# Kernel optimization log

Hardware: AMD Instinct MI355X
Metric: run time of the kernel (lower is better)

## Reference

```python
import jax, jax.numpy as jnp
import numpy as np

B, S, D, H, DFF, L, V = 256, 77, 512, 8, 2048, 12, 49408
HD = D // H
EPS = 1e-5


def setup_inputs() -> dict:
    key = jax.random.key(0)
    ks = jax.random.split(key, 12)
    s = 0.02
    n = lambda k, shape: s * jax.random.normal(k, shape, dtype=jnp.float32)
    return {
        "input_ids": jax.random.randint(ks[0], (B, S), 0, V),
        "attention_mask": jnp.ones((B, S), dtype=jnp.int32),
        "tok_emb": n(ks[1], (V, D)),
        "pos_emb": n(ks[2], (S, D)),
        "ln1_w": jnp.ones((L, D)), "ln1_b": jnp.zeros((L, D)),
        "q_w": n(ks[3], (L, D, D)), "q_b": jnp.zeros((L, D)),
        "k_w": n(ks[4], (L, D, D)), "k_b": jnp.zeros((L, D)),
        "v_w": n(ks[5], (L, D, D)), "v_b": jnp.zeros((L, D)),
        "o_w": n(ks[6], (L, D, D)), "o_b": jnp.zeros((L, D)),
        "ln2_w": jnp.ones((L, D)), "ln2_b": jnp.zeros((L, D)),
        "fc1_w": n(ks[7], (L, DFF, D)), "fc1_b": jnp.zeros((L, DFF)),
        "fc2_w": n(ks[8], (L, D, DFF)), "fc2_b": jnp.zeros((L, D)),
        "lnf_w": jnp.ones((D,)), "lnf_b": jnp.zeros((D,)),
    }


def layer_norm(x, w, b):
    mu = jnp.mean(x, axis=-1, keepdims=True)
    var = jnp.mean(jnp.square(x - mu), axis=-1, keepdims=True)
    return (x - mu) * jax.lax.rsqrt(var + EPS) * w + b


def quick_gelu(x):
    return x * jax.nn.sigmoid(1.702 * x)


def _encoder(x, mask, layer_params):
    scale = HD ** -0.5

    def heads(t):  # [B,S,D] -> [B,H,S,HD]
        return t.reshape(B, S, H, HD).transpose(0, 2, 1, 3)

    def layer(x, p):
        (ln1w, ln1b, qw, qb, kw, kb, vw, vb, ow, ob,
         ln2w, ln2b, f1w, f1b, f2w, f2b) = p
        h = layer_norm(x, ln1w, ln1b)
        q = heads((h @ qw.T + qb) * scale)
        k = heads(h @ kw.T + kb)
        v = heads(h @ vw.T + vb)
        scores = jnp.einsum('bhqd,bhkd->bhqk', q, k) + mask
        probs = jax.nn.softmax(scores, axis=-1)
        a = jnp.einsum('bhqk,bhkd->bhqd', probs, v)
        a = a.transpose(0, 2, 1, 3).reshape(B, S, D) @ ow.T + ob
        x = x + a
        h = layer_norm(x, ln2w, ln2b)
        h = quick_gelu(h @ f1w.T + f1b)
        h = h @ f2w.T + f2b
        return x + h, None

    x, _ = jax.lax.scan(layer, x, layer_params)
    return x


def reference(input_ids, attention_mask, tok_emb, pos_emb,
              ln1_w, ln1_b, q_w, q_b, k_w, k_b, v_w, v_b, o_w, o_b,
              ln2_w, ln2_b, fc1_w, fc1_b, fc2_w, fc2_b, lnf_w, lnf_b):
    x = tok_emb[input_ids] + pos_emb[None]
    neg = jnp.finfo(x.dtype).min
    causal = jnp.triu(jnp.full((S, S), neg, x.dtype), k=1)[None, None]  # [1,1,S,S]
    pad = (1.0 - attention_mask.astype(x.dtype))[:, None, None, :] * neg  # [B,1,1,S]
    mask = causal + pad  # [B,1,S,S]
    layer_params = (ln1_w, ln1_b, q_w, q_b, k_w, k_b, v_w, v_b, o_w, o_b,
                    ln2_w, ln2_b, fc1_w, fc1_b, fc2_w, fc2_b)
    x = _encoder(x, mask, layer_params)
    last_hidden = layer_norm(x, lnf_w, lnf_b)
    # pooled output: eot token = argmax of input_ids (CLIP convention)
    pooled = last_hidden[jnp.arange(B), jnp.argmax(input_ids, axis=-1)]
    return last_hidden, pooled
```

## Files before the change

kernel.cpp:

```cpp
#include <hip/hip_runtime.h>
#include <math.h>

constexpr int BATCH  = 256;
constexpr int SEQ    = 77;
constexpr int DMODEL = 512;
constexpr int NHEAD  = 8;
constexpr int DHEAD  = 64;
constexpr int DFF    = 2048;
constexpr int NLAYER = 12;
constexpr int NTOK   = BATCH * SEQ;
constexpr int NQKV   = 3 * DMODEL;
constexpr float NEGBIG = -3.402823466e38f;

typedef __attribute__((ext_vector_type(8))) short bf16x8;
typedef __attribute__((ext_vector_type(4))) float f32x4;
typedef __attribute__((ext_vector_type(8))) unsigned short u16x8;

typedef __attribute__((address_space(3))) unsigned char lds_u8;
typedef const __attribute__((address_space(1))) unsigned char g_u8;

__device__ __forceinline__ unsigned short f2bf(float f) {
    unsigned u = __float_as_uint(f);
    u = (u + 0x7FFF + ((u >> 16) & 1)) >> 16;
    return (unsigned short)u;
}

#define VMCNT4 asm volatile("s_waitcnt vmcnt(4)" ::: "memory")
#define LGKM0  asm volatile("s_waitcnt lgkmcnt(0)" ::: "memory")
#define SCHEDB __builtin_amdgcn_sched_barrier(0)
#define BARRIER do { SCHEDB; __builtin_amdgcn_s_barrier(); SCHEDB; } while (0)

__global__ __launch_bounds__(256) void conv_qkv_kernel(
    const float* __restrict__ qw, const float* __restrict__ kw,
    const float* __restrict__ vw, unsigned short* __restrict__ dst)
{
    int i4 = blockIdx.x * 256 + threadIdx.x;
    int e = i4 * 4;
    int l = e / (NQKV * DMODEL);
    int rem = e - l * (NQKV * DMODEL);
    int row = rem >> 9;
    int k   = rem & 511;
    const float* src;
    float scale = 1.0f;
    size_t lbase = (size_t)l * DMODEL * DMODEL;
    if (row < 512)       { src = qw + lbase + (size_t)row * DMODEL + k; scale = 0.125f; }
    else if (row < 1024) { src = kw + lbase + (size_t)(row - 512) * DMODEL + k; }
    else                 { src = vw + lbase + (size_t)(row - 1024) * DMODEL + k; }
    float4 v = *(const float4*)src;
    ushort4 o;
    o.x = f2bf(v.x * scale); o.y = f2bf(v.y * scale);
    o.z = f2bf(v.z * scale); o.w = f2bf(v.w * scale);
    *(ushort4*)&dst[e] = o;
}

__global__ __launch_bounds__(256) void conv_kernel(
    const float* __restrict__ src, unsigned short* __restrict__ dst)
{
    int e = (blockIdx.x * 256 + threadIdx.x) * 4;
    float4 v = *(const float4*)&src[e];
    ushort4 o;
    o.x = f2bf(v.x); o.y = f2bf(v.y); o.z = f2bf(v.z); o.w = f2bf(v.w);
    *(ushort4*)&dst[e] = o;
}

__global__ __launch_bounds__(256) void bias_qkv_kernel(
    const float* __restrict__ qb, const float* __restrict__ kb,
    const float* __restrict__ vb, float* __restrict__ dst)
{
    int e = blockIdx.x * 256 + threadIdx.x;
    int l = e / NQKV;
    int row = e - l * NQKV;
    float v;
    if (row < 512)       v = qb[l * DMODEL + row] * 0.125f;
    else if (row < 1024) v = kb[l * DMODEL + row - 512];
    else                 v = vb[l * DMODEL + row - 1024];
    dst[e] = v;
}

__global__ __launch_bounds__(256) void embed_kernel(
    const int* __restrict__ ids, const float* __restrict__ tok,
    const float* __restrict__ pos, float* __restrict__ x)
{
    int f = blockIdx.x * 256 + threadIdx.x;
    int total = NTOK * (DMODEL / 4);
    if (f >= total) return;
    int n  = f >> 7;
    int d4 = f & 127;
    int s  = n % SEQ;
    int id = ids[n];
    float4 t = *(const float4*)&tok[(size_t)id * DMODEL + d4 * 4];
    float4 p = *(const float4*)&pos[(size_t)s  * DMODEL + d4 * 4];
    float4 o; o.x = t.x + p.x; o.y = t.y + p.y; o.z = t.z + p.z; o.w = t.w + p.w;
    *(float4*)&x[(size_t)n * DMODEL + d4 * 4] = o;
}

template <bool BF16OUT>
__global__ __launch_bounds__(256) void ln_kernel(
    const float* __restrict__ x, const float* __restrict__ w,
    const float* __restrict__ b, void* __restrict__ out, int nrows)
{
    int row = blockIdx.x * 4 + (threadIdx.x >> 6);
    if (row >= nrows) return;
    int ln = threadIdx.x & 63;
    const float* xr = x + (size_t)row * DMODEL + ln * 8;
    float4 v0 = *(const float4*)xr;
    float4 v1 = *(const float4*)(xr + 4);
    float va[8] = {v0.x, v0.y, v0.z, v0.w, v1.x, v1.y, v1.z, v1.w};
    float sum = 0.f, sq = 0.f;
#pragma unroll
    for (int j = 0; j < 8; ++j) { sum += va[j]; sq = fmaf(va[j], va[j], sq); }
#pragma unroll
    for (int o = 32; o; o >>= 1) { sum += __shfl_xor(sum, o); sq += __shfl_xor(sq, o); }
    float mu  = sum * (1.0f / DMODEL);
    float var = sq * (1.0f / DMODEL) - mu * mu;
    var = fmaxf(var, 0.0f);
    float inv = 1.0f / sqrtf(var + 1e-5f);
    const float* wp = w + ln * 8;
    const float* bp = b + ln * 8;
    float o8[8];
#pragma unroll
    for (int j = 0; j < 8; ++j) o8[j] = (va[j] - mu) * inv * wp[j] + bp[j];
    if (BF16OUT) {
        u16x8 pk;
#pragma unroll
        for (int j = 0; j < 8; ++j) pk[j] = f2bf(o8[j]);
        *(u16x8*)((unsigned short*)out + (size_t)row * DMODEL + ln * 8) = pk;
    } else {
        float* op = (float*)out + (size_t)row * DMODEL + ln * 8;
        *(float4*)op       = make_float4(o8[0], o8[1], o8[2], o8[3]);
        *(float4*)(op + 4) = make_float4(o8[4], o8[5], o8[6], o8[7]);
    }
}

template <int MODE, bool OUTBF>
__global__ __launch_bounds__(512, 2) void gemm8_bf16(
    const unsigned short* __restrict__ A, const unsigned short* __restrict__ W,
    const float* __restrict__ bias, const float* __restrict__ R,
    void* __restrict__ Cout, int M, int N, int K, int gx)
{
    __shared__ __align__(16) char lds[131072];
    const int nwg = gridDim.x;
    const int wg  = blockIdx.x;
    const int q8  = nwg >> 3, r8 = nwg & 7;
    const int xcd = wg & 7, pos = wg >> 3;
    const int start = (xcd < r8) ? xcd * (q8 + 1) : r8 * (q8 + 1) + (xcd - r8) * q8;
    const int newid = start + pos;
    const int by = newid / gx;
    const int bx = newid - by * gx;
    const int m0 = by * 256;
    const int n0 = bx * 256;

    const int tid  = threadIdx.x;
    const int wid  = tid >> 6;
    const int lane = tid & 63;
    const int wr   = wid >> 2;
    const int wc   = wid & 3;
    const int lhi  = lane >> 4;
    const int llo  = lane & 15;

    const int srow  = tid >> 3;
    const int cglob = (tid & 7) ^ (srow & 7);
    const unsigned short* Ap = A + (size_t)(m0 + srow) * K + cglob * 8;
    const unsigned short* Wp = W + (size_t)(n0 + srow) * K + cglob * 8;
    const int NT  = K >> 6;
    const int NT2 = K >> 7;

    const int cb0 = ((0 * 4 + lhi) ^ (llo & 7)) * 16;
    const int cb1 = ((1 * 4 + lhi) ^ (llo & 7)) * 16;
    const int rbA0 = (wr * 128 + 0 * 64 + llo) * 128;
    const int rbA1 = (wr * 128 + 1 * 64 + llo) * 128;
    const int rbB0 = (wc * 64 + 0 * 32 + llo) * 128;
    const int rbB1 = (wc * 64 + 1 * 32 + llo) * 128;

    f32x4 acc[8][4];
#pragma unroll
    for (int i = 0; i < 8; ++i)
#pragma unroll
        for (int j = 0; j < 4; ++j) acc[i][j] = (f32x4){0.f, 0.f, 0.f, 0.f};

    bf16x8 am[4][2], bn0[2][2], bn1[2][2];

    auto stA = [&](int b, int h, int kt) {
#pragma unroll
        for (int i = h * 2; i < h * 2 + 2; ++i)
            __builtin_amdgcn_global_load_lds(
                (g_u8*)(Ap + (size_t)i * 64 * K + kt * 64),
                (lds_u8*)(lds + b * 32768 + i * 8192 + wid * 1024), 16, 0, 0);
    };
    auto stB = [&](int b, int h, int kt) {
#pragma unroll
        for (int i = h * 2; i < h * 2 + 2; ++i)
            __builtin_amdgcn_global_load_lds(
                (g_u8*)(Wp + (size_t)i * 64 * K + kt * 64),
                (lds_u8*)(lds + 65536 + b * 32768 + i * 8192 + wid * 1024), 16, 0, 0);
    };
    auto rdA = [&](int b, int mh) {
        int base = b * 32768 + (mh ? rbA1 : rbA0);
#pragma unroll
        for (int fm = 0; fm < 4; ++fm) {
            am[fm][0] = *(const bf16x8*)(lds + base + fm * 2048 + cb0);
            am[fm][1] = *(const bf16x8*)(lds + base + fm * 2048 + cb1);
        }
    };
    auto rdB = [&](int b, int nh, bf16x8 (&bn)[2][2]) {
        int base = 65536 + b * 32768 + (nh ? rbB1 : rbB0);
#pragma unroll
        for (int fn = 0; fn < 2; ++fn) {
            bn[fn][0] = *(const bf16x8*)(lds + base + fn * 2048 + cb0);
            bn[fn][1] = *(const bf16x8*)(lds + base + fn * 2048 + cb1);
        }
    };
    auto mq = [&](int mh, int nh, bf16x8 (&bn)[2][2]) {
        __builtin_amdgcn_s_setprio(1);
#pragma unroll
        for (int fm = 0; fm < 4; ++fm)
#pragma unroll
            for (int fn = 0; fn < 2; ++fn)
#pragma unroll
                for (int ks = 0; ks < 2; ++ks)
                    acc[mh * 4 + fm][nh * 2 + fn] =
                        __builtin_amdgcn_mfma_f32_16x16x32_bf16(
                            am[fm][ks], bn[fn][ks], acc[mh * 4 + fm][nh * 2 + fn], 0, 0, 0);
        __builtin_amdgcn_s_setprio(0);
    };

    stA(0, 0, 0); stA(0, 1, 0);
    stB(0, 0, 0); stB(0, 1, 0);
    stB(1, 0, 1); stB(1, 1, 1);
    VMCNT4;
    BARRIER;

    for (int it = 0; it < NT2; ++it) {
        const int k1 = 2 * it + 1;
        const int k2 = (2 * it + 2 < NT) ? 2 * it + 2 : NT - 1;
        const int k3 = (2 * it + 3 < NT) ? 2 * it + 3 : NT - 1;
        rdA(0, 0); rdB(0, 0, bn0);
        stA(1, 0, k1);
        LGKM0; BARRIER;
        mq(0, 0, bn0);
        rdB(0, 1, bn1);
        stA(1, 1, k1);
        LGKM0; BARRIER;
        mq(0, 1, bn1);
        rdA(0, 1);
        stB(0, 0, k2);
        LGKM0; BARRIER;
        mq(1, 1, bn1);
        stB(0, 1, k2);
        VMCNT4; BARRIER;
        mq(1, 0, bn0);
        rdA(1, 0); rdB(1, 0, bn0);
        stA(0, 0, k2);
        LGKM0; BARRIER;
        mq(0, 0, bn0);
        rdB(1, 1, bn1);
        stA(0, 1, k2);
        LGKM0; BARRIER;
        mq(0, 1, bn1);
        rdA(1, 1);
        stB(1, 0, k3);
        LGKM0; BARRIER;
        mq(1, 1, bn1);
        stB(1, 1, k3);
        VMCNT4; BARRIER;
        mq(1, 0, bn0);
    }

    if (OUTBF) {
        unsigned short* sb = (unsigned short*)lds;
#pragma unroll
        for (int j = 0; j < 4; ++j) {
            int colL = wc * 64 + j * 16 + llo;
            float bv = bias[n0 + colL];
#pragma unroll
            for (int i = 0; i < 8; ++i) {
                int rowL = wr * 128 + i * 16 + lhi * 4;
#pragma unroll
                for (int r = 0; r < 4; ++r) {
                    float o = acc[i][j][r] + bv;
                    if (MODE == 2) o = o / (1.0f + __expf(-1.702f * o));
                    sb[(rowL + r) * 256 + colL] = f2bf(o);
                }
            }
        }
        __syncthreads();
        const int l5 = lane & 31, lh2 = lane >> 5;
#pragma unroll
        for (int rr = 0; rr < 16; ++rr) {
            int rowL = rr * 16 + wid * 2 + lh2;
            u16x8 v = *(const u16x8*)&sb[rowL * 256 + l5 * 8];
            *(u16x8*)((unsigned short*)Cout + (size_t)(m0 + rowL) * N + n0 + l5 * 8) = v;
        }
    } else {
        float* sf = (float*)lds;
#pragma unroll
        for (int mh = 0; mh < 2; ++mh) {
            if (mh) __syncthreads();
            if (wr == mh) {
#pragma unroll
                for (int j = 0; j < 4; ++j) {
                    int colL = wc * 64 + j * 16 + llo;
                    float bv = bias[n0 + colL];
#pragma unroll
                    for (int i = 0; i < 8; ++i) {
                        int rowL = i * 16 + lhi * 4;
#pragma unroll
                        for (int r = 0; r < 4; ++r)
                            sf[(rowL + r) * 256 + colL] = acc[i][j][r] + bv;
                    }
                }
            }
            __syncthreads();
#pragma unroll
            for (int rr = 0; rr < 16; ++rr) {
                int rowL = rr * 8 + wid;
                size_t gidx = (size_t)(m0 + mh * 128 + rowL) * N + n0 + lane * 4;
                f32x4 v = *(const f32x4*)&sf[rowL * 256 + lane * 4];
                if (MODE == 3) {
                    f32x4 rv = *(const f32x4*)&R[gidx];
                    v = v + rv;
                }
                *(f32x4*)((float*)Cout + gidx) = v;
            }
        }
    }
}

__global__ __launch_bounds__(256) void attn_mfma_kernel(
    const unsigned short* __restrict__ qkv, const int* __restrict__ amask,
    unsigned short* __restrict__ out)
{
    const int bh = blockIdx.x;
    const int b = bh >> 3;
    const int h = bh & 7;
    __shared__ __align__(16) char smem[68160];
    char* Qs = smem;
    char* Ks = smem + 10240;
    char* Vt = smem;
    char* Pb = smem + 20480;
    float* ss = (float*)(smem + 40960);
    float* padm = (float*)(smem + 67840);
    const int tid  = threadIdx.x;
    const int wid  = tid >> 6;
    const int lane = tid & 63;
    const int llo  = lane & 15;
    const int lhi  = lane >> 4;

    for (int f = tid; f < 640; f += 256) {
        int r = f >> 3, c = f & 7;
        bf16x8 pq, pk;
        if (r < SEQ) {
            size_t g = ((size_t)(b * SEQ + r)) * NQKV + h * DHEAD + c * 8;
            pq = *(const bf16x8*)&qkv[g];
            pk = *(const bf16x8*)&qkv[g + 512];
        } else {
#pragma unroll
            for (int j = 0; j < 8; ++j) { pq[j] = 0; pk[j] = 0; }
        }
        int byte = r * 128 + ((c * 16) ^ ((r & 7) << 4));
        *(bf16x8*)(Qs + byte) = pq;
        *(bf16x8*)(Ks + byte) = pk;
    }
    for (int s = tid; s < SEQ; s += 256)
        padm[s] = (1.0f - (float)amask[b * SEQ + s]) * NEGBIG;
    __syncthreads();

    for (int t = wid; t < 25; t += 4) {
        int rt = t / 5, ct = t % 5;
        int ar = rt * 16 + llo;
        int br = ct * 16 + llo;
        int aswz = (ar & 7) << 4;
        int bswz = (br & 7) << 4;
        bf16x8 a0 = *(const bf16x8*)(Qs + ar * 128 + ((lhi * 16) ^ aswz));
        bf16x8 a1 = *(const bf16x8*)(Qs + ar * 128 + (((lhi + 4) * 16) ^ aswz));
        bf16x8 b0 = *(const bf16x8*)(Ks + br * 128 + ((lhi * 16) ^ bswz));
        bf16x8 b1 = *(const bf16x8*)(Ks + br * 128 + (((lhi + 4) * 16) ^ bswz));
        f32x4 acc = (f32x4){0.f, 0.f, 0.f, 0.f};
        acc = __builtin_amdgcn_mfma_f32_16x16x32_bf16(a0, b0, acc, 0, 0, 0);
        acc = __builtin_amdgcn_mfma_f32_16x16x32_bf16(a1, b1, acc, 0, 0, 0);
        int ki = ct * 16 + llo;
#pragma unroll
        for (int r = 0; r < 4; ++r) {
            int qi = rt * 16 + lhi * 4 + r;
            ss[qi * 84 + ki] = (ki > qi || ki >= SEQ) ? NEGBIG : (acc[r] + padm[ki]);
        }
    }
    __syncthreads();

    for (int f = tid; f < SEQ * 8; f += 256) {
        int s = f >> 3, d8 = (f & 7) * 8;
        bf16x8 v = *(const bf16x8*)&qkv[((size_t)(b * SEQ + s)) * NQKV + 1024 + h * DHEAD + d8];
        int chunk16 = (s >> 3) * 16, within = (s & 7) * 2;
#pragma unroll
        for (int j = 0; j < 8; ++j) {
            int d = d8 + j;
            int byte = d * 256 + (chunk16 ^ ((d & 7) << 4)) + within;
            *(short*)(Vt + byte) = v[j];
        }
    }
    for (int f = tid; f < 64 * 19; f += 256) {
        int d = f & 63, s = 77 + (f >> 6);
        int byte = d * 256 + (((s >> 3) * 16) ^ ((d & 7) << 4)) + (s & 7) * 2;
        *(short*)(Vt + byte) = 0;
    }

    for (int qi = wid; qi < SEQ; qi += 4) {
        float s0 = ss[qi * 84 + lane];
        float s1 = (lane < 16) ? ss[qi * 84 + 64 + lane] : NEGBIG;
        float m = fmaxf(s0, s1);
#pragma unroll
        for (int o = 32; o; o >>= 1) m = fmaxf(m, __shfl_xor(m, o));
        float e0 = __expf(s0 - m);
        float e1 = (lane < 16) ? __expf(s1 - m) : 0.f;
        float tsum = e0 + e1;
#pragma unroll
        for (int o = 32; o; o >>= 1) tsum += __shfl_xor(tsum, o);
        float rinv = 1.0f / tsum;
        int qswz = (qi & 7) << 4;
        {
            int col = lane;
            int byte = qi * 256 + (((col >> 3) * 16) ^ qswz) + (col & 7) * 2;
            *(short*)(Pb + byte) = (short)f2bf(e0 * rinv);
        }
        if (lane < 32) {
            int col = 64 + lane;
            float p = (lane < 16) ? e1 * rinv : 0.f;
            int byte = qi * 256 + (((col >> 3) * 16) ^ qswz) + (col & 7) * 2;
            *(short*)(Pb + byte) = (short)f2bf(p);
        }
    }
    __syncthreads();

    for (int t = wid; t < 20; t += 4) {
        int rt = t >> 2, ct = t & 3;
        int ar = rt * 16 + llo;
        int br = ct * 16 + llo;
        int aswz = (ar & 7) << 4;
        int bswz = (br & 7) << 4;
        f32x4 acc = (f32x4){0.f, 0.f, 0.f, 0.f};
#pragma unroll
        for (int kc = 0; kc < 3; ++kc) {
            bf16x8 af  = *(const bf16x8*)(Pb + ar * 256 + (((kc * 4 + lhi) * 16) ^ aswz));
            bf16x8 bf_ = *(const bf16x8*)(Vt + br * 256 + (((kc * 4 + lhi) * 16) ^ bswz));
            acc = __builtin_amdgcn_mfma_f32_16x16x32_bf16(af, bf_, acc, 0, 0, 0);
        }
        int d = ct * 16 + llo;
#pragma unroll
        for (int r = 0; r < 4; ++r) {
            int qi = rt * 16 + lhi * 4 + r;
            if (qi < SEQ)
                out[((size_t)(b * SEQ + qi)) * DMODEL + h * DHEAD + d] = f2bf(acc[r]);
        }
    }
}

__global__ __launch_bounds__(64) void pool_kernel(
    const int* __restrict__ ids, const float* __restrict__ lh,
    float* __restrict__ pooled)
{
    int b = blockIdx.x;
    int ln = threadIdx.x;
    __shared__ int sidx;
    if (ln == 0) {
        int best = ids[b * SEQ]; int bi = 0;
        for (int s = 1; s < SEQ; ++s) {
            int vv = ids[b * SEQ + s];
            if (vv > best) { best = vv; bi = s; }
        }
        sidx = bi;
    }
    __syncthreads();
    const float* src = lh + ((size_t)(b * SEQ + sidx)) * DMODEL + ln * 8;
    float* dst = pooled + (size_t)b * DMODEL + ln * 8;
    float4 a = *(const float4*)src;
    float4 c = *(const float4*)(src + 4);
    *(float4*)dst       = a;
    *(float4*)(dst + 4) = c;
}

extern "C" void kernel_launch(void* const* d_in, const int* in_sizes, int n_in,
                              void* d_out, int out_size, void* d_ws, size_t ws_size,
                              hipStream_t stream) {
    const int*   ids   = (const int*)d_in[0];
    const int*   amask = (const int*)d_in[1];
    const float* tok   = (const float*)d_in[2];
    const float* pos   = (const float*)d_in[3];
    const float* ln1w  = (const float*)d_in[4];
    const float* ln1b  = (const float*)d_in[5];
    const float* qw    = (const float*)d_in[6];
    const float* qbias = (const float*)d_in[7];
    const float* kw    = (const float*)d_in[8];
    const float* kbias = (const float*)d_in[9];
    const float* vw    = (const float*)d_in[10];
    const float* vbias = (const float*)d_in[11];
    const float* ow    = (const float*)d_in[12];
    const float* obias = (const float*)d_in[13];
    const float* ln2w  = (const float*)d_in[14];
    const float* ln2b  = (const float*)d_in[15];
    const float* f1w   = (const float*)d_in[16];
    const float* f1b   = (const float*)d_in[17];
    const float* f2w   = (const float*)d_in[18];
    const float* f2b   = (const float*)d_in[19];
    const float* lnfw  = (const float*)d_in[20];
    const float* lnfb  = (const float*)d_in[21];

    char* p = (char*)d_ws;
    float* x = (float*)p;                      p += (size_t)NTOK * DMODEL * 4;
    unsigned short* hbuf = (unsigned short*)p; p += (size_t)NTOK * DMODEL * 2;
    unsigned short* qkvb = (unsigned short*)p; p += (size_t)NTOK * NQKV * 2;
    unsigned short* ao = (unsigned short*)p;   p += (size_t)NTOK * DMODEL * 2;
    unsigned short* ff = (unsigned short*)p;   p += (size_t)NTOK * DFF * 2;
    unsigned short* wqkv = (unsigned short*)p; p += (size_t)NLAYER * NQKV * DMODEL * 2;
    unsigned short* wo   = (unsigned short*)p; p += (size_t)NLAYER * DMODEL * DMODEL * 2;
    unsigned short* wf1  = (unsigned short*)p; p += (size_t)NLAYER * DFF * DMODEL * 2;
    unsigned short* wf2  = (unsigned short*)p; p += (size_t)NLAYER * DMODEL * DFF * 2;
    float* bqkv = (float*)p;                   p += (size_t)NLAYER * NQKV * 4;

    conv_qkv_kernel<<<(NLAYER * NQKV * DMODEL / 4) / 256, 256, 0, stream>>>(qw, kw, vw, wqkv);
    conv_kernel<<<(NLAYER * DMODEL * DMODEL / 4) / 256, 256, 0, stream>>>(ow, wo);
    conv_kernel<<<(NLAYER * DFF * DMODEL / 4) / 256, 256, 0, stream>>>(f1w, wf1);
    conv_kernel<<<(NLAYER * DMODEL * DFF / 4) / 256, 256, 0, stream>>>(f2w, wf2);
    bias_qkv_kernel<<<(NLAYER * NQKV) / 256, 256, 0, stream>>>(qbias, kbias, vbias, bqkv);

    embed_kernel<<<(NTOK * (DMODEL / 4) + 255) / 256, 256, 0, stream>>>(ids, tok, pos, x);

    const int MB = NTOK / 256;
    dim3 gqkv(MB * (NQKV / 256));
    dim3 g512(MB * (DMODEL / 256));
    dim3 g2048(MB * (DFF / 256));

    for (int l = 0; l < NLAYER; ++l) {
        const size_t wD2 = (size_t)l * DMODEL * DMODEL;
        const size_t wDF = (size_t)l * DFF * DMODEL;
        const size_t oD  = (size_t)l * DMODEL;
        const size_t oF  = (size_t)l * DFF;

        ln_kernel<true><<<NTOK / 4, 256, 0, stream>>>(x, ln1w + oD, ln1b + oD, hbuf, NTOK);
        gemm8_bf16<0, true><<<gqkv, 512, 0, stream>>>(
            hbuf, wqkv + (size_t)l * NQKV * DMODEL, bqkv + (size_t)l * NQKV, nullptr,
            qkvb, NTOK, NQKV, DMODEL, NQKV / 256);
        attn_mfma_kernel<<<BATCH * NHEAD, 256, 0, stream>>>(qkvb, amask, ao);
        gemm8_bf16<3, false><<<g512, 512, 0, stream>>>(
            ao, wo + wD2, obias + oD, x, x, NTOK, DMODEL, DMODEL, DMODEL / 256);
        ln_kernel<true><<<NTOK / 4, 256, 0, stream>>>(x, ln2w + oD, ln2b + oD, hbuf, NTOK);
        gemm8_bf16<2, true><<<g2048, 512, 0, stream>>>(
            hbuf, wf1 + wDF, f1b + oF, nullptr, ff, NTOK, DFF, DMODEL, DFF / 256);
        gemm8_bf16<3, false><<<g512, 512, 0, stream>>>(
            ff, wf2 + wDF, f2b + oD, x, x, NTOK, DMODEL, DFF, DMODEL / 256);
    }

    float* outf = (float*)d_out;
    ln_kernel<false><<<NTOK / 4, 256, 0, stream>>>(x, lnfw, lnfb, outf, NTOK);
    pool_kernel<<<BATCH, 64, 0, stream>>>(ids, outf, outf + (size_t)NTOK * DMODEL);
}
```

Before: 3.759 ms.

## Prefetch V into registers early and widen softmax to four rows per wave

The attention kernel now issues the global loads for the V head slice at kernel entry into registers, so their latency overlaps the Q/K staging and the QK^T MFMA phase. The loads are written into the transposed LDS layout only after the score barrier. The softmax now handles four rows per wave, with 16 lanes per row and five columns per lane, which cuts the shuffle reductions per row. The explicit zeroing of V padding rows is replaced by zeroing the padded P columns 80-95 instead. This relies on the stale LDS contents under Vt staying finite, and it raises register pressure from holding three V vectors across the first phase.

```diff
diff --git a/kernel.cpp b/kernel.cpp
--- a/kernel.cpp
+++ b/kernel.cpp
@@ -346,6 +346,24 @@
     const int llo  = lane & 15;
     const int lhi  = lane >> 4;
 
+    const size_t vbase = ((size_t)(b * SEQ)) * NQKV + 1024 + h * DHEAD;
+    bf16x8 vr0, vr1, vr2;
+    {
+        int c0 = tid, c1 = tid + 256, c2 = tid + 512;
+        vr0 = *(const bf16x8*)&qkv[vbase + (size_t)(c0 >> 3) * NQKV + (c0 & 7) * 8];
+        vr1 = *(const bf16x8*)&qkv[vbase + (size_t)(c1 >> 3) * NQKV + (c1 & 7) * 8];
+        if (c2 < 616)
+            vr2 = *(const bf16x8*)&qkv[vbase + (size_t)(c2 >> 3) * NQKV + (c2 & 7) * 8];
+    }
+
+    if (tid < 160) {
+        int r = tid >> 1, ch = 10 + (tid & 1);
+        bf16x8 z;
+#pragma unroll
+        for (int j = 0; j < 8; ++j) z[j] = 0;
+        *(bf16x8*)(Pb + r * 256 + ((ch ^ (r & 7)) * 16)) = z;
+    }
+
     for (int f = tid; f < 640; f += 256) {
         int r = f >> 3, c = f & 7;
         bf16x8 pq, pk;
@@ -387,46 +405,50 @@
     }
     __syncthreads();
 
-    for (int f = tid; f < SEQ * 8; f += 256) {
-        int s = f >> 3, d8 = (f & 7) * 8;
-        bf16x8 v = *(const bf16x8*)&qkv[((size_t)(b * SEQ + s)) * NQKV + 1024 + h * DHEAD + d8];
-        int chunk16 = (s >> 3) * 16, within = (s & 7) * 2;
-#pragma unroll
-        for (int j = 0; j < 8; ++j) {
-            int d = d8 + j;
-            int byte = d * 256 + (chunk16 ^ ((d & 7) << 4)) + within;
-            *(short*)(Vt + byte) = v[j];
-        }
-    }
-    for (int f = tid; f < 64 * 19; f += 256) {
-        int d = f & 63, s = 77 + (f >> 6);
-        int byte = d * 256 + (((s >> 3) * 16) ^ ((d & 7) << 4)) + (s & 7) * 2;
-        *(short*)(Vt + byte) = 0;
-    }
-
-    for (int qi = wid; qi < SEQ; qi += 4) {
-        float s0 = ss[qi * 84 + lane];
-        float s1 = (lane < 16) ? ss[qi * 84 + 64 + lane] : NEGBIG;
-        float m = fmaxf(s0, s1);
-#pragma unroll
-        for (int o = 32; o; o >>= 1) m = fmaxf(m, __shfl_xor(m, o));
-        float e0 = __expf(s0 - m);
-        float e1 = (lane < 16) ? __expf(s1 - m) : 0.f;
-        float tsum = e0 + e1;
-#pragma unroll
-        for (int o = 32; o; o >>= 1) tsum += __shfl_xor(tsum, o);
-        float rinv = 1.0f / tsum;
-        int qswz = (qi & 7) << 4;
-        {
-            int col = lane;
-            int byte = qi * 256 + (((col >> 3) * 16) ^ qswz) + (col & 7) * 2;
-            *(short*)(Pb + byte) = (short)f2bf(e0 * rinv);
-        }
-        if (lane < 32) {
-            int col = 64 + lane;
-            float p = (lane < 16) ? e1 * rinv : 0.f;
-            int byte = qi * 256 + (((col >> 3) * 16) ^ qswz) + (col & 7) * 2;
-            *(short*)(Pb + byte) = (short)f2bf(p);
+    {
+        auto writeV = [&](int c, bf16x8 v) {
+            int s = c >> 3, d8 = (c & 7) * 8;
+            int chunk16 = (s >> 3) * 16, within = (s & 7) * 2;
+#pragma unroll
+            for (int j = 0; j < 8; ++j) {
+                int d = d8 + j;
+                *(short*)(Vt + d * 256 + (chunk16 ^ ((d & 7) << 4)) + within) = v[j];
+            }
+        };
+        writeV(tid, vr0);
+        writeV(tid + 256, vr1);
+        if (tid + 512 < 616) writeV(tid + 512, vr2);
+    }
+
+    {
+        const int g = lane >> 4;
+        const int c = lane & 15;
+#pragma unroll
+        for (int pass = 0; pass < 5; ++pass) {
+            int r = pass * 16 + wid * 4 + g;
+            float v0 = ss[r * 84 + c];
+            float v1 = ss[r * 84 + c + 16];
+            float v2 = ss[r * 84 + c + 32];
+            float v3 = ss[r * 84 + c + 48];
+            float v4 = ss[r * 84 + c + 64];
+            float m = fmaxf(fmaxf(fmaxf(v0, v1), fmaxf(v2, v3)), v4);
+#pragma unroll
+            for (int o = 8; o; o >>= 1) m = fmaxf(m, __shfl_xor(m, o));
+            float e0 = __expf(v0 - m), e1 = __expf(v1 - m), e2 = __expf(v2 - m);
+            float e3 = __expf(v3 - m), e4 = __expf(v4 - m);
+            float tsum = e0 + e1 + e2 + e3 + e4;
+#pragma unroll
+            for (int o = 8; o; o >>= 1) tsum += __shfl_xor(tsum, o);
+            float rinv = 1.0f / tsum;
+            int rswz = (r & 7) << 4;
+            int rb = r * 256;
+            float ev[5] = {e0, e1, e2, e3, e4};
+#pragma unroll
+            for (int i = 0; i < 5; ++i) {
+                int col = c + i * 16;
+                *(short*)(Pb + rb + (((col >> 3) * 16) ^ rswz) + (col & 7) * 2) =
+                    (short)f2bf(ev[i] * rinv);
+            }
         }
     }
     __syncthreads();
```

Measured after the change: 3.319 ms. 1.13x faster.
